# Optimization experiments

Hardware: AMD Instinct MI355X
Metric: run time of the kernel (lower is better)

## Reference

```python
import jax, jax.numpy as jnp
import numpy as np

B, S, D, H = 1, 2048, 2048, 16
HD = D // H
I = 8192
EPS = 1e-5
NEG = -1e9


def setup_inputs() -> dict:
    key = jax.random.key(0)
    ks = jax.random.split(key, 9)
    x = jax.random.normal(ks[0], (B, S, D), jnp.float32)
    # causal additive mask
    causal = jnp.triu(jnp.full((S, S), NEG, jnp.float32), k=1)[None, None]
    # RoPE tables (duplicated-half convention matching rotate_half)
    inv_freq = 1.0 / (10000.0 ** (np.arange(0, HD, 2, dtype=np.float32) / HD))
    t = np.arange(S, dtype=np.float32)
    freqs = np.outer(t, inv_freq)  # [S, HD/2]
    emb = np.concatenate([freqs, freqs], axis=-1)  # [S, HD]
    freqs_cos = jnp.asarray(np.cos(emb))[None, None]  # [1,1,S,HD]
    freqs_sin = jnp.asarray(np.sin(emb))[None, None]
    scale = 0.02
    return {
        "x": x,
        "attention_mask": causal,
        "freqs_cos": freqs_cos,
        "freqs_sin": freqs_sin,
        "wq": jax.random.normal(ks[1], (D, D), jnp.float32) * scale,
        "wk": jax.random.normal(ks[2], (D, D), jnp.float32) * scale,
        "wv": jax.random.normal(ks[3], (D, D), jnp.float32) * scale,
        "wo": jax.random.normal(ks[4], (D, D), jnp.float32) * scale,
        "w1": jax.random.normal(ks[5], (D, I), jnp.float32) * scale,
        "w2": jax.random.normal(ks[6], (I, D), jnp.float32) * scale,
        "w3": jax.random.normal(ks[7], (D, I), jnp.float32) * scale,
        "attn_norm_w": jnp.ones((D,), jnp.float32),
        "ffn_norm_w": jnp.ones((D,), jnp.float32),
    }


def rms_norm(x, w):
    xf = x.astype(jnp.float32)
    n = xf * jax.lax.rsqrt(jnp.mean(xf * xf, axis=-1, keepdims=True) + EPS)
    return w * n.astype(x.dtype)


def rotate_half(x):
    x1, x2 = jnp.split(x, 2, axis=-1)
    return jnp.concatenate([-x2, x1], axis=-1)


def reference(x, attention_mask, freqs_cos, freqs_sin, wq, wk, wv, wo, w1, w2, w3, attn_norm_w, ffn_norm_w):
    nx = rms_norm(x, attn_norm_w)
    # project and split heads -> [B, H, S, HD]
    def heads(y, w):
        return (y @ w).reshape(B, S, H, HD).transpose(0, 2, 1, 3)
    q = heads(nx, wq)
    k = heads(nx, wk)
    v = heads(nx, wv)
    q = q * freqs_cos + rotate_half(q) * freqs_sin
    k = k * freqs_cos + rotate_half(k) * freqs_sin
    scores = jnp.einsum("bhqd,bhkd->bhqk", q, k) / jnp.sqrt(jnp.float32(HD))
    scores = scores + attention_mask
    attn = jax.nn.softmax(scores, axis=-1)
    out = jnp.einsum("bhqk,bhkd->bhqd", attn, v)
    out = out.transpose(0, 2, 1, 3).reshape(B, S, D) @ wo
    x = x + out
    nx = rms_norm(x, ffn_norm_w)
    ff = (jax.nn.silu(nx @ w1) * (nx @ w3)) @ w2
    return x + ff
```

## Files before the change

### kernel.cpp

```cpp
#include <hip/hip_runtime.h>

typedef unsigned short u16;
typedef __bf16 bf16_t;
typedef bf16_t bf16x8 __attribute__((ext_vector_type(8)));
typedef float f32x4 __attribute__((ext_vector_type(4)));

#define D_MODEL 2048
#define SEQ     2048
#define NHEAD   16
#define HDIM    128
#define IDIM    8192
#define QKV_LD  6144

__device__ __forceinline__ u16 f2bf(float f) {
    unsigned u = __float_as_uint(f);
    u += 0x7fffu + ((u >> 16) & 1u);
    return (u16)(u >> 16);
}
__device__ __forceinline__ float bf2f(u16 u) {
    return __uint_as_float(((unsigned)u) << 16);
}
__device__ __forceinline__ void gload16(const void* g, void* l) {
    __builtin_amdgcn_global_load_lds(
        (const __attribute__((address_space(1))) unsigned int*)g,
        (__attribute__((address_space(3))) unsigned int*)l, 16, 0, 0);
}
#define MFMA16(a, b, c) __builtin_amdgcn_mfma_f32_16x16x32_bf16((a), (b), (c), 0, 0, 0)

__global__ __launch_bounds__(256) void rmsnorm_kernel(
    const float* __restrict__ x, const float* __restrict__ w, u16* __restrict__ out)
{
    int row = blockIdx.x, t = threadIdx.x;
    const float4* xr = (const float4*)(x + (size_t)row * D_MODEL);
    float4 a = xr[t * 2], b = xr[t * 2 + 1];
    float ss = a.x*a.x + a.y*a.y + a.z*a.z + a.w*a.w
             + b.x*b.x + b.y*b.y + b.z*b.z + b.w*b.w;
#pragma unroll
    for (int off = 32; off > 0; off >>= 1) ss += __shfl_down(ss, off, 64);
    __shared__ float red[4];
    __shared__ float sinv;
    if ((t & 63) == 0) red[t >> 6] = ss;
    __syncthreads();
    if (t == 0) sinv = rsqrtf((red[0] + red[1] + red[2] + red[3]) * (1.0f / D_MODEL) + 1e-5f);
    __syncthreads();
    float inv = sinv;
    const float4* w4 = (const float4*)w;
    float4 wa = w4[t * 2], wb = w4[t * 2 + 1];
    u16* o = out + (size_t)row * D_MODEL + t * 8;
    o[0] = f2bf(a.x * inv * wa.x); o[1] = f2bf(a.y * inv * wa.y);
    o[2] = f2bf(a.z * inv * wa.z); o[3] = f2bf(a.w * inv * wa.w);
    o[4] = f2bf(b.x * inv * wb.x); o[5] = f2bf(b.y * inv * wb.y);
    o[6] = f2bf(b.z * inv * wb.z); o[7] = f2bf(b.w * inv * wb.w);
}

__global__ __launch_bounds__(256) void tcvt_kernel(
    const float* __restrict__ src, u16* __restrict__ dst, int R, int C)
{
    __shared__ float tile[32][33];
    int tx = threadIdx.x & 31, ty = threadIdx.x >> 5;
    int c = blockIdx.x * 32 + tx;
    int rb = blockIdx.y * 32;
#pragma unroll
    for (int i = 0; i < 32; i += 8)
        tile[ty + i][tx] = src[(size_t)(rb + ty + i) * C + c];
    __syncthreads();
    int dr = blockIdx.x * 32 + ty;
    int dc = rb + tx;
#pragma unroll
    for (int i = 0; i < 32; i += 8)
        dst[(size_t)(dr + i) * R + dc] = f2bf(tile[tx][ty + i]);
}

__global__ __launch_bounds__(256) void tbf16_kernel(
    const u16* __restrict__ src, u16* __restrict__ dst, int R, int C, int ld)
{
    __shared__ u16 tile[32][34];
    int tx = threadIdx.x & 31, ty = threadIdx.x >> 5;
    int c = blockIdx.x * 32 + tx;
    int rb = blockIdx.y * 32;
#pragma unroll
    for (int i = 0; i < 32; i += 8)
        tile[ty + i][tx] = src[(size_t)(rb + ty + i) * ld + c];
    __syncthreads();
    int dr = blockIdx.x * 32 + ty;
    int dc = rb + tx;
#pragma unroll
    for (int i = 0; i < 32; i += 8)
        dst[(size_t)(dr + i) * R + dc] = tile[tx][ty + i];
}

__global__ __launch_bounds__(256) void rope_kernel(
    u16* __restrict__ qkv, const float* __restrict__ fc, const float* __restrict__ fs)
{
    int s = blockIdx.x, t = threadIdx.x;
    const float* cr = fc + (size_t)s * HDIM;
    const float* sr = fs + (size_t)s * HDIM;
#pragma unroll
    for (int p = 0; p < 4; p++) {
        int pi = p * 256 + t;
        int h = pi >> 6, d = pi & 63;
        size_t base = (size_t)s * QKV_LD + h * HDIM + d;
        float c1 = cr[d], s1 = sr[d], c2 = cr[d + 64], s2 = sr[d + 64];
        float q1 = bf2f(qkv[base]), q2 = bf2f(qkv[base + 64]);
        qkv[base]      = f2bf(q1 * c1 - q2 * s1);
        qkv[base + 64] = f2bf(q2 * c2 + q1 * s2);
        size_t kb = base + 2048;
        float k1 = bf2f(qkv[kb]), k2 = bf2f(qkv[kb + 64]);
        qkv[kb]      = f2bf(k1 * c1 - k2 * s1);
        qkv[kb + 64] = f2bf(k2 * c2 + k1 * s2);
    }
}

template <int BM, int EPI>
__global__ __launch_bounds__(256, 3) void gemm_bt(
    const u16* __restrict__ A, const u16* __restrict__ Bt,
    const float* __restrict__ res, const u16* __restrict__ gate,
    float* __restrict__ outf, u16* __restrict__ outb,
    int M, int N, int K, int lda, int ldb)
{
    constexpr int WC = (BM == 128) ? 2 : 4;
    constexpr int MI = 4;
    constexpr int NJ = (BM == 128) ? 4 : 2;
    constexpr int LA = BM / 64;
    __shared__ __align__(16) u16 lA[BM * 32];
    __shared__ __align__(16) u16 lB[128 * 32];
    int t = threadIdx.x;
    int wave = t >> 6, lane = t & 63, quad = lane >> 4, l16 = lane & 15;
    int wr = wave / WC, wc = wave % WC;
    int m0 = blockIdx.y * BM, n0 = blockIdx.x * 128;
    int mb = wr * (MI * 16), nb = wc * (NJ * 16);
    int koff = blockIdx.z * K;

    f32x4 acc[MI][NJ];
    const f32x4 fzero = {0.f, 0.f, 0.f, 0.f};
#pragma unroll
    for (int i = 0; i < MI; i++)
#pragma unroll
        for (int j = 0; j < NJ; j++) acc[i][j] = fzero;

    const u16* gA[LA]; u16* lAp[LA];
#pragma unroll
    for (int l = 0; l < LA; l++) {
        int row = l * 64 + (t >> 2);
        int gch = (t & 3) ^ ((row >> 1) & 3);
        gA[l] = A + (size_t)(m0 + row) * lda + koff + gch * 8;
        lAp[l] = &lA[(l * 256 + t) * 8];
    }
    const u16* gB[2]; u16* lBp[2];
#pragma unroll
    for (int l = 0; l < 2; l++) {
        int row = l * 64 + (t >> 2);
        int gch = (t & 3) ^ ((row >> 1) & 3);
        gB[l] = Bt + (size_t)(n0 + row) * ldb + koff + gch * 8;
        lBp[l] = &lB[(l * 256 + t) * 8];
    }
    int fslot = (quad ^ ((l16 >> 1) & 3)) * 8;

    for (int k0 = 0; k0 < K; k0 += 32) {
#pragma unroll
        for (int l = 0; l < LA; l++) gload16(gA[l] + k0, lAp[l]);
        gload16(gB[0] + k0, lBp[0]);
        gload16(gB[1] + k0, lBp[1]);
        asm volatile("s_waitcnt vmcnt(0)" ::: "memory");
        __syncthreads();
        bf16x8 af[MI], bfv[NJ];
#pragma unroll
        for (int i = 0; i < MI; i++)
            af[i] = *(const bf16x8*)&lA[(mb + i * 16 + l16) * 32 + fslot];
#pragma unroll
        for (int j = 0; j < NJ; j++)
            bfv[j] = *(const bf16x8*)&lB[(nb + j * 16 + l16) * 32 + fslot];
#pragma unroll
        for (int i = 0; i < MI; i++)
#pragma unroll
            for (int j = 0; j < NJ; j++)
                acc[i][j] = MFMA16(af[i], bfv[j], acc[i][j]);
        __syncthreads();
    }

    float* po = (EPI == 3) ? outf + (size_t)blockIdx.z * M * N : outf;
#pragma unroll
    for (int i = 0; i < MI; i++)
#pragma unroll
        for (int j = 0; j < NJ; j++)
#pragma unroll
            for (int r = 0; r < 4; r++) {
                int m = m0 + mb + i * 16 + quad * 4 + r;
                int n = n0 + nb + j * 16 + l16;
                size_t idx = (size_t)m * N + n;
                float v = acc[i][j][r];
                if (EPI == 0) {
                    outb[idx] = f2bf(v);
                } else if (EPI == 1) {
                    outf[idx] = res[idx] + v;
                } else if (EPI == 2) {
                    float g = bf2f(gate[idx]);
                    outb[idx] = f2bf(g / (1.f + __expf(-g)) * v);
                } else {
                    po[idx] = v;
                }
            }
}

__global__ __launch_bounds__(256) void reduce4_kernel(
    const float* __restrict__ x1, const float* __restrict__ part, float* __restrict__ out)
{
    size_t i = (size_t)blockIdx.x * 256 + threadIdx.x;
    float4 a = ((const float4*)x1)[i];
#pragma unroll
    for (int z = 0; z < 4; z++) {
        float4 pv = ((const float4*)(part + (size_t)z * SEQ * D_MODEL))[i];
        a.x += pv.x; a.y += pv.y; a.z += pv.z; a.w += pv.w;
    }
    ((float4*)out)[i] = a;
}

__global__ __launch_bounds__(256, 1) void attn_kernel(
    const u16* __restrict__ q, const u16* __restrict__ k,
    const u16* __restrict__ vt, u16* __restrict__ ctx)
{
    __shared__ __align__(16) u16 sK[2][128 * 128];
    __shared__ __align__(16) u16 sV[128 * 128];
    __shared__ __align__(16) u16 sP[4][16 * 32 * 8];

    int t = threadIdx.x;
    int wave = t >> 6, lane = t & 63, quad = lane >> 4, l16 = lane & 15;
    int h = blockIdx.y, qt = blockIdx.x;
    int q0 = qt * 128;
    int srow = t >> 4, schunk = t & 15;

#pragma unroll
    for (int p = 0; p < 8; p++) {
        int r = p * 16 + srow;
        int gc = schunk ^ (r & 7);
        gload16(q + (size_t)(q0 + r) * QKV_LD + h * HDIM + gc * 8, &sK[1][p * 2048 + t * 8]);
    }
#pragma unroll
    for (int p = 0; p < 8; p++) {
        int r = p * 16 + srow;
        int gc = schunk ^ (r & 7);
        gload16(k + (size_t)r * QKV_LD + h * HDIM + gc * 8, &sK[0][p * 2048 + t * 8]);
    }
    asm volatile("s_waitcnt vmcnt(0)" ::: "memory");
    __builtin_amdgcn_s_barrier();
    __builtin_amdgcn_sched_barrier(0);

    bf16x8 qa[2][4];
#pragma unroll
    for (int i = 0; i < 2; i++) {
        int row = wave * 32 + i * 16 + l16;
#pragma unroll
        for (int kk = 0; kk < 4; kk++)
            qa[i][kk] = *(const bf16x8*)&sK[1][row * 128 + (((kk * 4 + quad) ^ (row & 7)) * 8)];
    }
    asm volatile("s_waitcnt lgkmcnt(0)" ::: "memory");
    __builtin_amdgcn_sched_barrier(0);
    __builtin_amdgcn_s_barrier();
    __builtin_amdgcn_sched_barrier(0);

    const float scale = 0.08838834764831845f;
    float m_r[2][4], l_r[2][4];
#pragma unroll
    for (int i = 0; i < 2; i++)
#pragma unroll
        for (int r = 0; r < 4; r++) { m_r[i][r] = -3e38f; l_r[i][r] = 0.f; }
    const f32x4 fzero = {0.f, 0.f, 0.f, 0.f};
    f32x4 o[2][8];
#pragma unroll
    for (int i = 0; i < 2; i++)
#pragma unroll
        for (int j = 0; j < 8; j++) o[i][j] = fzero;
    u16* sPw = sP[wave];

    for (int kt = 0; kt <= qt; kt++) {
        int c = kt & 1;
        int k0 = kt * 128;

#pragma unroll
        for (int p = 0; p < 8; p++) {
            int r = p * 16 + srow;
            int gc = schunk ^ (r & 7);
            gload16(vt + (size_t)(h * HDIM + r) * SEQ + k0 + gc * 8, &sV[p * 2048 + t * 8]);
        }
        if (kt < qt) {
            int k1 = k0 + 128;
#pragma unroll
            for (int p = 0; p < 8; p++) {
                int r = p * 16 + srow;
                int gc = schunk ^ (r & 7);
                gload16(k + (size_t)(k1 + r) * QKV_LD + h * HDIM + gc * 8,
                        &sK[1 - c][p * 2048 + t * 8]);
            }
            asm volatile("s_waitcnt vmcnt(16)" ::: "memory");
        } else {
            asm volatile("s_waitcnt vmcnt(8)" ::: "memory");
        }
        __builtin_amdgcn_sched_barrier(0);
        __builtin_amdgcn_s_barrier();
        __builtin_amdgcn_sched_barrier(0);

        f32x4 sc[2][8];
#pragma unroll
        for (int i = 0; i < 2; i++)
#pragma unroll
            for (int j = 0; j < 8; j++) sc[i][j] = fzero;
        const u16* sKc = sK[c];
#pragma unroll
        for (int kk = 0; kk < 4; kk++) {
            bf16x8 kf[8];
#pragma unroll
            for (int j = 0; j < 8; j++)
                kf[j] = *(const bf16x8*)&sKc[(j * 16 + l16) * 128 +
                                             (((kk * 4 + quad) ^ (l16 & 7)) * 8)];
#pragma unroll
            for (int i = 0; i < 2; i++)
#pragma unroll
                for (int j = 0; j < 8; j++)
                    sc[i][j] = MFMA16(qa[i][kk], kf[j], sc[i][j]);
        }

#pragma unroll
        for (int i = 0; i < 2; i++)
#pragma unroll
            for (int j = 0; j < 8; j++) sc[i][j] = sc[i][j] * scale;
        if (kt == qt) {
#pragma unroll
            for (int i = 0; i < 2; i++)
#pragma unroll
                for (int j = 0; j < 8; j++) {
                    int col = j * 16 + l16;
#pragma unroll
                    for (int r = 0; r < 4; r++) {
                        int row = wave * 32 + i * 16 + quad * 4 + r;
                        if (col > row) sc[i][j][r] = -3e38f;
                    }
                }
        }

#pragma unroll
        for (int i = 0; i < 2; i++)
#pragma unroll
            for (int r = 0; r < 4; r++) {
                float mx = sc[i][0][r];
#pragma unroll
                for (int j = 1; j < 8; j++) mx = fmaxf(mx, sc[i][j][r]);
#pragma unroll
                for (int d = 1; d < 16; d <<= 1) mx = fmaxf(mx, __shfl_xor(mx, d, 64));
                float mo = m_r[i][r];
                float mn = fmaxf(mo, mx);
                float al = __expf(mo - mn);
                m_r[i][r] = mn;
                float s = 0.f;
#pragma unroll
                for (int j = 0; j < 8; j++) {
                    float pv = __expf(sc[i][j][r] - mn);
                    sc[i][j][r] = pv;
                    s += pv;
                }
#pragma unroll
                for (int d = 1; d < 16; d <<= 1) s += __shfl_xor(s, d, 64);
                l_r[i][r] = al * l_r[i][r] + s;
#pragma unroll
                for (int j = 0; j < 8; j++) o[i][j][r] *= al;
                int rl = i * 16 + quad * 4 + r;
#pragma unroll
                for (int j = 0; j < 8; j++) {
                    int col = j * 16 + l16;
                    sPw[(col >> 3) * 256 + rl * 8 + (col & 7)] = f2bf(sc[i][j][r]);
                }
            }

        if (kt < qt) {
            asm volatile("s_waitcnt vmcnt(8) lgkmcnt(0)" ::: "memory");
        } else {
            asm volatile("s_waitcnt vmcnt(0) lgkmcnt(0)" ::: "memory");
        }
        __builtin_amdgcn_sched_barrier(0);
        __builtin_amdgcn_s_barrier();
        __builtin_amdgcn_sched_barrier(0);

#pragma unroll
        for (int kk = 0; kk < 4; kk++) {
            bf16x8 pa[2], vf[8];
#pragma unroll
            for (int i = 0; i < 2; i++)
                pa[i] = *(const bf16x8*)&sPw[(kk * 4 + quad) * 256 + (i * 16 + l16) * 8];
#pragma unroll
            for (int j = 0; j < 8; j++)
                vf[j] = *(const bf16x8*)&sV[(j * 16 + l16) * 128 +
                                            (((kk * 4 + quad) ^ (l16 & 7)) * 8)];
#pragma unroll
            for (int i = 0; i < 2; i++)
#pragma unroll
                for (int j = 0; j < 8; j++)
                    o[i][j] = MFMA16(pa[i], vf[j], o[i][j]);
        }
        asm volatile("s_waitcnt lgkmcnt(0)" ::: "memory");
        __builtin_amdgcn_sched_barrier(0);
        __builtin_amdgcn_s_barrier();
        __builtin_amdgcn_sched_barrier(0);
    }

#pragma unroll
    for (int i = 0; i < 2; i++)
#pragma unroll
        for (int r = 0; r < 4; r++) {
            int row = wave * 32 + i * 16 + quad * 4 + r;
            float inv = 1.f / l_r[i][r];
#pragma unroll
            for (int j = 0; j < 8; j++) {
                int n = h * HDIM + j * 16 + l16;
                ctx[(size_t)(q0 + row) * D_MODEL + n] = f2bf(o[i][j][r] * inv);
            }
        }
}

extern "C" void kernel_launch(void* const* d_in, const int* in_sizes, int n_in,
                              void* d_out, int out_size, void* d_ws, size_t ws_size,
                              hipStream_t stream)
{
    const float* x    = (const float*)d_in[0];
    const float* fcos = (const float*)d_in[2];
    const float* fsin = (const float*)d_in[3];
    const float* wq   = (const float*)d_in[4];
    const float* wk   = (const float*)d_in[5];
    const float* wv   = (const float*)d_in[6];
    const float* wo   = (const float*)d_in[7];
    const float* w1   = (const float*)d_in[8];
    const float* w2   = (const float*)d_in[9];
    const float* w3   = (const float*)d_in[10];
    const float* anw  = (const float*)d_in[11];
    const float* fnw  = (const float*)d_in[12];
    float* out = (float*)d_out;

    const size_t MB = 1024 * 1024;
    char* base = (char*)d_ws;
    u16*   qkvT = (u16*)  (base + 0);
    u16*   woT  = (u16*)  (base + 24 * MB);
    u16*   w1T  = (u16*)  (base + 32 * MB);
    u16*   w3T  = (u16*)  (base + 64 * MB);
    u16*   w2T  = (u16*)  (base + 96 * MB);
    u16*   nx   = (u16*)  (base + 128 * MB);
    u16*   qkv  = (u16*)  (base + 136 * MB);
    u16*   vtb  = (u16*)  (base + 160 * MB);
    u16*   ctxb = (u16*)  (base + 168 * MB);
    float* x1   = (float*)(base + 176 * MB);
    u16*   nx2  = (u16*)  (base + 192 * MB);
    u16*   h1b  = (u16*)  (base + 200 * MB);
    u16*   hb   = (u16*)  (base + 232 * MB);
    float* part = (float*)(base + 0);

    dim3 blk(256);

    rmsnorm_kernel<<<SEQ, blk, 0, stream>>>(x, anw, nx);
    tcvt_kernel<<<dim3(64, 64),  blk, 0, stream>>>(wq, qkvT,                       D_MODEL, D_MODEL);
    tcvt_kernel<<<dim3(64, 64),  blk, 0, stream>>>(wk, qkvT + 2048 * 2048,         D_MODEL, D_MODEL);
    tcvt_kernel<<<dim3(64, 64),  blk, 0, stream>>>(wv, qkvT + (size_t)4096 * 2048, D_MODEL, D_MODEL);
    tcvt_kernel<<<dim3(64, 64),  blk, 0, stream>>>(wo, woT, D_MODEL, D_MODEL);
    tcvt_kernel<<<dim3(256, 64), blk, 0, stream>>>(w1, w1T, D_MODEL, IDIM);
    tcvt_kernel<<<dim3(256, 64), blk, 0, stream>>>(w3, w3T, D_MODEL, IDIM);
    tcvt_kernel<<<dim3(64, 256), blk, 0, stream>>>(w2, w2T, IDIM, D_MODEL);

    gemm_bt<128, 0><<<dim3(48, 16), blk, 0, stream>>>(
        nx, qkvT, nullptr, nullptr, nullptr, qkv, SEQ, QKV_LD, D_MODEL, D_MODEL, D_MODEL);

    rope_kernel<<<SEQ, blk, 0, stream>>>(qkv, fcos, fsin);
    tbf16_kernel<<<dim3(64, 64), blk, 0, stream>>>(qkv + 4096, vtb, SEQ, D_MODEL, QKV_LD);

    attn_kernel<<<dim3(16, 16), blk, 0, stream>>>(qkv, qkv + 2048, vtb, ctxb);

    gemm_bt<64, 1><<<dim3(16, 32), blk, 0, stream>>>(
        ctxb, woT, x, nullptr, x1, nullptr, SEQ, D_MODEL, D_MODEL, D_MODEL, D_MODEL);

    rmsnorm_kernel<<<SEQ, blk, 0, stream>>>(x1, fnw, nx2);

    gemm_bt<128, 0><<<dim3(64, 16), blk, 0, stream>>>(
        nx2, w1T, nullptr, nullptr, nullptr, h1b, SEQ, IDIM, D_MODEL, D_MODEL, D_MODEL);
    gemm_bt<128, 2><<<dim3(64, 16), blk, 0, stream>>>(
        nx2, w3T, nullptr, h1b, nullptr, hb, SEQ, IDIM, D_MODEL, D_MODEL, D_MODEL);

    gemm_bt<128, 3><<<dim3(16, 16, 4), blk, 0, stream>>>(
        hb, w2T, nullptr, nullptr, part, nullptr, SEQ, D_MODEL, 2048, IDIM, IDIM);
    reduce4_kernel<<<dim3(4096), blk, 0, stream>>>(x1, part, out);
}
```

Baseline: 788.3 us.

## Add 256x256-tile 512-thread GEMM with XCD swizzle for QKV and FFN

Adds a new GEMM kernel that computes 256x256 output tiles with 8 waves, double-buffered LDS loads via global_load_lds, an XOR-swizzled LDS layout, s_setprio around the MFMA bursts, and a workgroup remap that spreads neighbouring tiles across XCDs. It replaces the 128-tile GEMM for the QKV projection, the w1/w3 FFN projections and the split-K w2 GEMM. The larger tiles raise arithmetic intensity and cut global and LDS traffic per FLOP. In exchange the grids become much smaller (e.g. 192 or 256 workgroups), which risks wave quantization and poorer occupancy on a 256-CU part, and the kernel needs 128 KB of LDS per block.

```diff
diff --git a/kernel.cpp b/kernel.cpp
--- a/kernel.cpp
+++ b/kernel.cpp
@@ -26,6 +26,8 @@
         (__attribute__((address_space(3))) unsigned int*)l, 16, 0, 0);
 }
 #define MFMA16(a, b, c) __builtin_amdgcn_mfma_f32_16x16x32_bf16((a), (b), (c), 0, 0, 0)
+#define VMCNT(n) asm volatile("s_waitcnt vmcnt(" #n ")" ::: "memory")
+#define SBAR() do { __builtin_amdgcn_sched_barrier(0); __builtin_amdgcn_s_barrier(); __builtin_amdgcn_sched_barrier(0); } while (0)
 
 __global__ __launch_bounds__(256) void rmsnorm_kernel(
     const float* __restrict__ x, const float* __restrict__ w, u16* __restrict__ out)
@@ -202,6 +204,142 @@
             }
 }
 
+template <int EPI>
+__global__ __launch_bounds__(512, 2) void gemm256(
+    const u16* __restrict__ A, const u16* __restrict__ Bt,
+    const u16* __restrict__ gate, float* __restrict__ outf, u16* __restrict__ outb,
+    int M, int N, int K, int lda, int ldb)
+{
+    __shared__ __align__(16) u16 sA[2][256 * 64];
+    __shared__ __align__(16) u16 sB[2][256 * 64];
+    int tid = threadIdx.x;
+    int lane = tid & 63, quad = lane >> 4, l16 = lane & 15;
+    int wave = tid >> 6, wm = wave >> 2, wn = wave & 3;
+    int x8 = l16 & 7;
+
+    int nbn = gridDim.x, nbm = gridDim.y;
+    int nwg = nbn * nbm;
+    int nb = blockIdx.y * nbn + blockIdx.x;
+    int q8 = nwg >> 3;
+    int sw = (nb & 7) * q8 + (nb >> 3);
+    int m0 = (sw % nbm) * 256, n0 = (sw / nbm) * 256;
+    size_t koff = (size_t)blockIdx.z * K;
+
+    int srow = tid >> 3, slot = tid & 7;
+    const u16* gA[2][2]; const u16* gB[2][2];
+#pragma unroll
+    for (int h = 0; h < 2; h++)
+#pragma unroll
+        for (int l = 0; l < 2; l++) {
+            int row = h * 128 + l * 64 + srow;
+            int gch = slot ^ (row & 7);
+            gA[h][l] = A + (size_t)(m0 + row) * lda + koff + gch * 8;
+            gB[h][l] = Bt + (size_t)(n0 + row) * ldb + koff + gch * 8;
+        }
+
+    f32x4 acc[8][4];
+    const f32x4 fzero = {0.f, 0.f, 0.f, 0.f};
+#pragma unroll
+    for (int i = 0; i < 8; i++)
+#pragma unroll
+        for (int j = 0; j < 4; j++) acc[i][j] = fzero;
+
+#define ISSUE_TILE(KOFF, AD, BD)                                               \
+    gload16(gA[0][0] + (KOFF), (AD) + tid * 8);                                \
+    gload16(gA[0][1] + (KOFF), (AD) + 4096 + tid * 8);                         \
+    gload16(gA[1][0] + (KOFF), (AD) + 8192 + tid * 8);                         \
+    gload16(gA[1][1] + (KOFF), (AD) + 12288 + tid * 8);                        \
+    gload16(gB[0][0] + (KOFF), (BD) + tid * 8);                                \
+    gload16(gB[0][1] + (KOFF), (BD) + 4096 + tid * 8);                         \
+    gload16(gB[1][0] + (KOFF), (BD) + 8192 + tid * 8);                         \
+    gload16(gB[1][1] + (KOFF), (BD) + 12288 + tid * 8);
+
+#define READ_A(MH)                                                             \
+    _Pragma("unroll")                                                          \
+    for (int mi = 0; mi < 4; mi++)                                             \
+        _Pragma("unroll")                                                      \
+        for (int kk = 0; kk < 2; kk++)                                         \
+            af[mi][kk] = *(const bf16x8*)&sac[(wm * 128 + (MH) * 64 + mi * 16 + l16) * 64 \
+                                              + (((kk * 4 + quad) ^ x8) * 8)];
+#define READ_B(BF, NH)                                                         \
+    _Pragma("unroll")                                                          \
+    for (int nj = 0; nj < 2; nj++)                                             \
+        _Pragma("unroll")                                                      \
+        for (int kk = 0; kk < 2; kk++)                                         \
+            BF[nj][kk] = *(const bf16x8*)&sbc[(wn * 64 + (NH) * 32 + nj * 16 + l16) * 64 \
+                                              + (((kk * 4 + quad) ^ x8) * 8)];
+#define QUAD_MFMA(BF, IOFF, JOFF)                                              \
+    __builtin_amdgcn_s_setprio(1);                                             \
+    _Pragma("unroll")                                                          \
+    for (int kk = 0; kk < 2; kk++)                                             \
+        _Pragma("unroll")                                                      \
+        for (int mi = 0; mi < 4; mi++)                                         \
+            _Pragma("unroll")                                                  \
+            for (int nj = 0; nj < 2; nj++)                                     \
+                acc[(IOFF) + mi][(JOFF) + nj] =                                \
+                    MFMA16(af[mi][kk], BF[nj][kk], acc[(IOFF) + mi][(JOFF) + nj]); \
+    __builtin_amdgcn_s_setprio(0);
+
+    ISSUE_TILE(0, sA[0], sB[0])
+    VMCNT(0);
+    SBAR();
+
+    int nk = K >> 6;
+    for (int t = 0; t < nk; ++t) {
+        int c = t & 1;
+        const u16* sac = sA[c]; const u16* sbc = sB[c];
+        bool pf = (t + 1 < nk);
+
+        if (pf) {
+            int kn = (t + 1) << 6;
+            u16* sad = sA[c ^ 1]; u16* sbd = sB[c ^ 1];
+            ISSUE_TILE(kn, sad, sbd)
+            VMCNT(8);
+        } else {
+            VMCNT(0);
+        }
+        SBAR();
+
+        bf16x8 af[4][2], bf0[2][2], bf1[2][2];
+        READ_A(0)
+        READ_B(bf0, 0)
+        READ_B(bf1, 1)
+        QUAD_MFMA(bf0, 0, 0)
+        QUAD_MFMA(bf1, 0, 2)
+        READ_A(1)
+        QUAD_MFMA(bf0, 4, 0)
+        QUAD_MFMA(bf1, 4, 2)
+
+        asm volatile("s_waitcnt lgkmcnt(0)" ::: "memory");
+        SBAR();
+    }
+#undef ISSUE_TILE
+#undef READ_A
+#undef READ_B
+#undef QUAD_MFMA
+
+    float* po = (EPI == 3) ? outf + (size_t)blockIdx.z * M * N : outf;
+#pragma unroll
+    for (int i = 0; i < 8; i++)
+#pragma unroll
+        for (int j = 0; j < 4; j++)
+#pragma unroll
+            for (int r = 0; r < 4; r++) {
+                int m = m0 + wm * 128 + (i >> 2) * 64 + (i & 3) * 16 + quad * 4 + r;
+                int n = n0 + wn * 64 + (j >> 1) * 32 + (j & 1) * 16 + l16;
+                size_t idx = (size_t)m * N + n;
+                float v = acc[i][j][r];
+                if (EPI == 0) {
+                    outb[idx] = f2bf(v);
+                } else if (EPI == 2) {
+                    float g = bf2f(gate[idx]);
+                    outb[idx] = f2bf(g / (1.f + __expf(-g)) * v);
+                } else {
+                    po[idx] = v;
+                }
+            }
+}
+
 __global__ __launch_bounds__(256) void reduce4_kernel(
     const float* __restrict__ x1, const float* __restrict__ part, float* __restrict__ out)
 {
@@ -451,6 +589,7 @@
     float* part = (float*)(base + 0);
 
     dim3 blk(256);
+    dim3 blk512(512);
 
     rmsnorm_kernel<<<SEQ, blk, 0, stream>>>(x, anw, nx);
     tcvt_kernel<<<dim3(64, 64),  blk, 0, stream>>>(wq, qkvT,                       D_MODEL, D_MODEL);
@@ -461,8 +600,8 @@
     tcvt_kernel<<<dim3(256, 64), blk, 0, stream>>>(w3, w3T, D_MODEL, IDIM);
     tcvt_kernel<<<dim3(64, 256), blk, 0, stream>>>(w2, w2T, IDIM, D_MODEL);
 
-    gemm_bt<128, 0><<<dim3(48, 16), blk, 0, stream>>>(
-        nx, qkvT, nullptr, nullptr, nullptr, qkv, SEQ, QKV_LD, D_MODEL, D_MODEL, D_MODEL);
+    gemm256<0><<<dim3(24, 8), blk512, 0, stream>>>(
+        nx, qkvT, nullptr, nullptr, qkv, SEQ, QKV_LD, D_MODEL, D_MODEL, D_MODEL);
 
     rope_kernel<<<SEQ, blk, 0, stream>>>(qkv, fcos, fsin);
     tbf16_kernel<<<dim3(64, 64), blk, 0, stream>>>(qkv + 4096, vtb, SEQ, D_MODEL, QKV_LD);
@@ -474,12 +613,12 @@
 
     rmsnorm_kernel<<<SEQ, blk, 0, stream>>>(x1, fnw, nx2);
 
-    gemm_bt<128, 0><<<dim3(64, 16), blk, 0, stream>>>(
-        nx2, w1T, nullptr, nullptr, nullptr, h1b, SEQ, IDIM, D_MODEL, D_MODEL, D_MODEL);
-    gemm_bt<128, 2><<<dim3(64, 16), blk, 0, stream>>>(
-        nx2, w3T, nullptr, h1b, nullptr, hb, SEQ, IDIM, D_MODEL, D_MODEL, D_MODEL);
-
-    gemm_bt<128, 3><<<dim3(16, 16, 4), blk, 0, stream>>>(
-        hb, w2T, nullptr, nullptr, part, nullptr, SEQ, D_MODEL, 2048, IDIM, IDIM);
+    gemm256<0><<<dim3(32, 8), blk512, 0, stream>>>(
+        nx2, w1T, nullptr, nullptr, h1b, SEQ, IDIM, D_MODEL, D_MODEL, D_MODEL);
+    gemm256<2><<<dim3(32, 8), blk512, 0, stream>>>(
+        nx2, w3T, h1b, nullptr, hb, SEQ, IDIM, D_MODEL, D_MODEL, D_MODEL);
+
+    gemm256<3><<<dim3(8, 8, 4), blk512, 0, stream>>>(
+        hb, w2T, nullptr, part, nullptr, SEQ, D_MODEL, D_MODEL, IDIM, IDIM);
     reduce4_kernel<<<dim3(4096), blk, 0, stream>>>(x1, part, out);
 }
```

Measured after the change: 803.0 us. No clear change (+1.9%).
